# Kernel optimization log

Hardware: AMD Instinct MI355X
Metric: run time of the kernel (lower is better)

## Reference

```python
import jax, jax.numpy as jnp
import numpy as np

MARGIN = 1.0
EPS = 1e-08


def setup_inputs() -> dict:
    key = jax.random.key(0)
    k0, k1 = jax.random.split(key)
    kernels0 = jax.random.normal(k0, (2048, 3, 3), dtype=jnp.float32)
    kernels1 = jax.random.normal(k1, (1024, 5, 5), dtype=jnp.float32)
    return {"kernels0": kernels0, "kernels1": kernels1}


def _layer_loss(kernels):
    n, d, _ = kernels.shape
    # Frobenius-normalize each kernel
    norms = jnp.sqrt(jnp.sum(kernels * kernels, axis=(1, 2), keepdims=True)) + EPS
    kn = kernels / norms                      # (n, d, d)
    inv = jnp.linalg.inv(kn)                  # (n, d, d)
    # AB[i, j] = inv[i] @ kn[j]; BA[i, j] = inv[j] @ kn[i]
    ab = jnp.einsum('iab,jbc->ijac', inv, kn)  # (n, n, d, d)
    ba = jnp.einsum('jab,ibc->ijac', inv, kn)  # (n, n, d, d)
    eye = jnp.eye(d, dtype=kernels.dtype)
    diff_ab = jnp.sqrt(jnp.sum((eye - ab) ** 2, axis=(2, 3)))  # (n, n)
    diff_ba = jnp.sqrt(jnp.sum((eye - ba) ** 2, axis=(2, 3)))  # (n, n)
    combined = jnp.tril(diff_ab) + jnp.triu(diff_ba)
    loss_mat = jax.nn.relu(MARGIN - combined)
    mask = ~jnp.eye(n, dtype=bool)
    loss_mat = jnp.where(mask, loss_mat, 0.0)
    return jnp.sum(loss_mat) / (n * (n - 1))


def reference(kernels0, kernels1):
    losses = [_layer_loss(kernels0), _layer_loss(kernels1)]
    return sum(losses) / len(losses)
```

## Files before the change

kernel.cpp:

```cpp
#include <hip/hip_runtime.h>
#include <math.h>

#define N0 2048
#define N1 1024
#define T0 128
#define T1 64
#define M0 (N0 / T0)
#define M1 (N1 / T1)
#define NB0 (M0 * (M0 + 1) / 2)
#define NB1 (M1 * (M1 + 1) / 2)
#define NBTOT (NB0 + NB1)


__device__ __forceinline__ void inv3_newton(const float* __restrict__ src, float* __restrict__ out) {
    float a[9];
    float ss = 0.0f;
#pragma unroll
    for (int e = 0; e < 9; ++e) { a[e] = src[e]; ss = fmaf(a[e], a[e], ss); }
    float rn = 1.0f / (sqrtf(ss) + 1e-8f);
#pragma unroll
    for (int e = 0; e < 9; ++e) a[e] *= rn;
    float c00 = a[4] * a[8] - a[5] * a[7];
    float c01 = -(a[3] * a[8] - a[5] * a[6]);
    float c02 = a[3] * a[7] - a[4] * a[6];
    float det = a[0] * c00 + a[1] * c01 + a[2] * c02;
    float id = 1.0f / det;
    float x[9];
    x[0] = c00 * id;
    x[1] = (a[2] * a[7] - a[1] * a[8]) * id;
    x[2] = (a[1] * a[5] - a[2] * a[4]) * id;
    x[3] = c01 * id;
    x[4] = (a[0] * a[8] - a[2] * a[6]) * id;
    x[5] = (a[2] * a[3] - a[0] * a[5]) * id;
    x[6] = c02 * id;
    x[7] = (a[1] * a[6] - a[0] * a[7]) * id;
    x[8] = (a[0] * a[4] - a[1] * a[3]) * id;
    float r[9];
#pragma unroll
    for (int i = 0; i < 3; ++i)
#pragma unroll
        for (int j = 0; j < 3; ++j) {
            float m = a[i * 3 + 0] * x[j];
            m = fmaf(a[i * 3 + 1], x[3 + j], m);
            m = fmaf(a[i * 3 + 2], x[6 + j], m);
            r[i * 3 + j] = ((i == j) ? 2.0f : 0.0f) - m;
        }
#pragma unroll
    for (int i = 0; i < 3; ++i)
#pragma unroll
        for (int j = 0; j < 3; ++j) {
            float m = x[i * 3 + 0] * r[j];
            m = fmaf(x[i * 3 + 1], r[3 + j], m);
            m = fmaf(x[i * 3 + 2], r[6 + j], m);
            out[i * 3 + j] = m;
        }
}

__device__ __forceinline__ void norm3(const float* __restrict__ src, float* __restrict__ out) {
    float a[9];
    float ss = 0.0f;
#pragma unroll
    for (int e = 0; e < 9; ++e) { a[e] = src[e]; ss = fmaf(a[e], a[e], ss); }
    float rn = 1.0f / (sqrtf(ss) + 1e-8f);
#pragma unroll
    for (int e = 0; e < 9; ++e) out[e] = a[e] * rn;
}

__device__ __forceinline__ void inv5_newton(const float* __restrict__ src, float* __restrict__ out) {
    float A[5][5], B[5][5], K[5][5];
    float ss = 0.0f;
#pragma unroll
    for (int r = 0; r < 5; ++r)
#pragma unroll
        for (int c = 0; c < 5; ++c) {
            float v = src[r * 5 + c];
            A[r][c] = v;
            ss = fmaf(v, v, ss);
        }
    float rn = 1.0f / (sqrtf(ss) + 1e-8f);
#pragma unroll
    for (int r = 0; r < 5; ++r)
#pragma unroll
        for (int c = 0; c < 5; ++c) {
            A[r][c] *= rn;
            K[r][c] = A[r][c];
            B[r][c] = (r == c) ? 1.0f : 0.0f;
        }
#pragma unroll
    for (int k = 0; k < 5; ++k) {
#pragma unroll
        for (int r = k + 1; r < 5; ++r) {
            bool sw = fabsf(A[r][k]) > fabsf(A[k][k]);
#pragma unroll
            for (int c = k; c < 5; ++c) {
                float Ar = A[r][c], Ak = A[k][c];
                A[r][c] = sw ? Ak : Ar;
                A[k][c] = sw ? Ar : Ak;
            }
#pragma unroll
            for (int c = 0; c < 5; ++c) {
                float Br = B[r][c], Bk = B[k][c];
                B[r][c] = sw ? Bk : Br;
                B[k][c] = sw ? Br : Bk;
            }
        }
        float piv = 1.0f / A[k][k];
#pragma unroll
        for (int c = k; c < 5; ++c) A[k][c] *= piv;
#pragma unroll
        for (int c = 0; c < 5; ++c) B[k][c] *= piv;
#pragma unroll
        for (int r = 0; r < 5; ++r) {
            if (r == k) continue;
            float f = A[r][k];
#pragma unroll
            for (int c = k; c < 5; ++c) A[r][c] = fmaf(-f, A[k][c], A[r][c]);
#pragma unroll
            for (int c = 0; c < 5; ++c) B[r][c] = fmaf(-f, B[k][c], B[r][c]);
        }
    }
    float R[5][5];
#pragma unroll
    for (int i = 0; i < 5; ++i)
#pragma unroll
        for (int j = 0; j < 5; ++j) {
            float m = K[i][0] * B[0][j];
#pragma unroll
            for (int k = 1; k < 5; ++k) m = fmaf(K[i][k], B[k][j], m);
            R[i][j] = ((i == j) ? 2.0f : 0.0f) - m;
        }
#pragma unroll
    for (int i = 0; i < 5; ++i)
#pragma unroll
        for (int j = 0; j < 5; ++j) {
            float m = B[i][0] * R[0][j];
#pragma unroll
            for (int k = 1; k < 5; ++k) m = fmaf(B[i][k], R[k][j], m);
            out[i * 5 + j] = m;
        }
}

__device__ __forceinline__ void norm5(const float* __restrict__ src, float* __restrict__ out) {
    float a[25];
    float ss = 0.0f;
#pragma unroll
    for (int e = 0; e < 25; ++e) { a[e] = src[e]; ss = fmaf(a[e], a[e], ss); }
    float rn = 1.0f / (sqrtf(ss) + 1e-8f);
#pragma unroll
    for (int e = 0; e < 25; ++e) out[e] = a[e] * rn;
}

__device__ __forceinline__ void tri_decode(int t, int& bi, int& bj) {
    bi = (int)((sqrtf(8.0f * t + 1.0f) - 1.0f) * 0.5f);
    while ((bi + 1) * (bi + 2) / 2 <= t) ++bi;
    while (bi * (bi + 1) / 2 > t) --bi;
    bj = t - bi * (bi + 1) / 2;
}

__global__ __launch_bounds__(256) void fused_kernel(const float* __restrict__ k0,
                                                    const float* __restrict__ k1,
                                                    float* __restrict__ out) {
    __shared__ float sA[1600];
    __shared__ float sB[1600];
    int tid = threadIdx.x;
    float contrib = 0.0f;
    bool isL0 = blockIdx.x < NB0;

    if (isL0) {
        int bi, bj;
        tri_decode(blockIdx.x, bi, bj);
        if (tid < 128) {
            inv3_newton(&k0[(bi * T0 + tid) * 9], &sA[tid * 9]);
        } else {
            int m = tid - 128;
            norm3(&k0[(bj * T0 + m) * 9], &sB[m * 9]);
        }
        __syncthreads();

        int ty = tid >> 4, tx = tid & 15;
        int ibase = bi * T0 + ty * 8, jbase = bj * T0 + tx * 8;
        float a[8][9];
#pragma unroll
        for (int u = 0; u < 8; ++u)
#pragma unroll
            for (int e = 0; e < 9; ++e) a[u][e] = sA[(ty * 8 + u) * 9 + e];
#pragma unroll
        for (int v = 0; v < 8; ++v) {
            float b[9];
#pragma unroll
            for (int e = 0; e < 9; ++e) b[e] = sB[(tx * 8 + v) * 9 + e];
#pragma unroll
            for (int u = 0; u < 8; ++u) {
                float s = 0.0f;
#pragma unroll
                for (int r = 0; r < 3; ++r)
#pragma unroll
                    for (int c = 0; c < 3; ++c) {
                        float m = a[u][r * 3 + 0] * b[c];
                        m = fmaf(a[u][r * 3 + 1], b[3 + c], m);
                        m = fmaf(a[u][r * 3 + 2], b[6 + c], m);
                        float d = ((r == c) ? 1.0f : 0.0f) - m;
                        s = fmaf(d, d, s);
                    }
                bool take = ((ibase + u) > (jbase + v)) && (s < 1.0f);
                contrib += take ? (1.0f - sqrtf(s)) : 0.0f;
            }
        }
    } else {
        int bi, bj;
        tri_decode(blockIdx.x - NB0, bi, bj);
        if (tid < 64) {
            inv5_newton(&k1[(bi * T1 + tid) * 25], &sA[tid * 25]);
        } else if (tid < 128) {
            int m = tid - 64;
            norm5(&k1[(bj * T1 + m) * 25], &sB[m * 25]);
        }
        __syncthreads();

        int ty = tid >> 4, tx = tid & 15;
        int ibase = bi * T1 + ty * 4, jbase = bj * T1 + tx * 4;
        float a[4][25];
#pragma unroll
        for (int u = 0; u < 4; ++u)
#pragma unroll
            for (int e = 0; e < 25; ++e) a[u][e] = sA[(ty * 4 + u) * 25 + e];
#pragma unroll
        for (int v = 0; v < 4; ++v) {
            float b[25];
#pragma unroll
            for (int e = 0; e < 25; ++e) b[e] = sB[(tx * 4 + v) * 25 + e];
#pragma unroll
            for (int u = 0; u < 4; ++u) {
                float s = 0.0f;
#pragma unroll
                for (int r = 0; r < 5; ++r)
#pragma unroll
                    for (int c = 0; c < 5; ++c) {
                        float m = a[u][r * 5 + 0] * b[c];
#pragma unroll
                        for (int k = 1; k < 5; ++k) m = fmaf(a[u][r * 5 + k], b[k * 5 + c], m);
                        float d = ((r == c) ? 1.0f : 0.0f) - m;
                        s = fmaf(d, d, s);
                    }
                bool take = ((ibase + u) > (jbase + v)) && (s < 1.0f);
                contrib += take ? (1.0f - sqrtf(s)) : 0.0f;
            }
        }
    }

#pragma unroll
    for (int off = 32; off; off >>= 1) contrib += __shfl_down(contrib, off);
    __shared__ float wsum[4];
    if ((tid & 63) == 0) wsum[tid >> 6] = contrib;
    __syncthreads();
    if (tid == 0) {
        double part = (double)(wsum[0] + wsum[1] + wsum[2] + wsum[3]);
        double scale = isL0 ? 1.0 / ((double)N0 * (double)(N0 - 1))
                            : 1.0 / ((double)N1 * (double)(N1 - 1));
        unsafeAtomicAdd(out, (float)(part * scale));
    }
}

extern "C" void kernel_launch(void* const* d_in, const int* in_sizes, int n_in,
                              void* d_out, int out_size, void* d_ws, size_t ws_size,
                              hipStream_t stream) {
    const float* k0 = (const float*)d_in[0];
    const float* k1 = (const float*)d_in[1];
    float* out = (float*)d_out;
    (void)d_ws; (void)ws_size;

    fused_kernel<<<NBTOT, 256, 0, stream>>>(k0, k1, out);
}
```

Baseline: 71.80 us.

## Precompute normalized kernels and inverses in a prep kernel; stride tile rows

Kernel normalization and inversion move out of the pairwise kernel into a separate prep kernel that writes normalized kernels and inverses to workspace once. Each pair block then only copies its tiles into shared memory, instead of recomputing the Newton-refined inverse for its row tile on every block. The per-thread row and column mapping also changes from contiguous groups of 8 or 4 to a stride of 16, which alters the shared-memory bank access pattern. The cost is an extra kernel launch and a global-memory round trip for the precomputed data.

Measured after the change: 75.73 us. 1.05x slower.

```diff
diff --git a/kernel.cpp b/kernel.cpp
--- a/kernel.cpp
+++ b/kernel.cpp
@@ -12,142 +12,134 @@
 #define NBTOT (NB0 + NB1)
 
 
-__device__ __forceinline__ void inv3_newton(const float* __restrict__ src, float* __restrict__ out) {
-    float a[9];
-    float ss = 0.0f;
-#pragma unroll
-    for (int e = 0; e < 9; ++e) { a[e] = src[e]; ss = fmaf(a[e], a[e], ss); }
-    float rn = 1.0f / (sqrtf(ss) + 1e-8f);
-#pragma unroll
-    for (int e = 0; e < 9; ++e) a[e] *= rn;
-    float c00 = a[4] * a[8] - a[5] * a[7];
-    float c01 = -(a[3] * a[8] - a[5] * a[6]);
-    float c02 = a[3] * a[7] - a[4] * a[6];
-    float det = a[0] * c00 + a[1] * c01 + a[2] * c02;
-    float id = 1.0f / det;
-    float x[9];
-    x[0] = c00 * id;
-    x[1] = (a[2] * a[7] - a[1] * a[8]) * id;
-    x[2] = (a[1] * a[5] - a[2] * a[4]) * id;
-    x[3] = c01 * id;
-    x[4] = (a[0] * a[8] - a[2] * a[6]) * id;
-    x[5] = (a[2] * a[3] - a[0] * a[5]) * id;
-    x[6] = c02 * id;
-    x[7] = (a[1] * a[6] - a[0] * a[7]) * id;
-    x[8] = (a[0] * a[4] - a[1] * a[3]) * id;
-    float r[9];
-#pragma unroll
-    for (int i = 0; i < 3; ++i)
-#pragma unroll
-        for (int j = 0; j < 3; ++j) {
-            float m = a[i * 3 + 0] * x[j];
-            m = fmaf(a[i * 3 + 1], x[3 + j], m);
-            m = fmaf(a[i * 3 + 2], x[6 + j], m);
-            r[i * 3 + j] = ((i == j) ? 2.0f : 0.0f) - m;
-        }
-#pragma unroll
-    for (int i = 0; i < 3; ++i)
-#pragma unroll
-        for (int j = 0; j < 3; ++j) {
-            float m = x[i * 3 + 0] * r[j];
-            m = fmaf(x[i * 3 + 1], r[3 + j], m);
-            m = fmaf(x[i * 3 + 2], r[6 + j], m);
-            out[i * 3 + j] = m;
-        }
-}
-
-__device__ __forceinline__ void norm3(const float* __restrict__ src, float* __restrict__ out) {
-    float a[9];
-    float ss = 0.0f;
-#pragma unroll
-    for (int e = 0; e < 9; ++e) { a[e] = src[e]; ss = fmaf(a[e], a[e], ss); }
-    float rn = 1.0f / (sqrtf(ss) + 1e-8f);
-#pragma unroll
-    for (int e = 0; e < 9; ++e) out[e] = a[e] * rn;
-}
-
-__device__ __forceinline__ void inv5_newton(const float* __restrict__ src, float* __restrict__ out) {
-    float A[5][5], B[5][5], K[5][5];
-    float ss = 0.0f;
-#pragma unroll
-    for (int r = 0; r < 5; ++r)
-#pragma unroll
-        for (int c = 0; c < 5; ++c) {
-            float v = src[r * 5 + c];
-            A[r][c] = v;
-            ss = fmaf(v, v, ss);
-        }
-    float rn = 1.0f / (sqrtf(ss) + 1e-8f);
-#pragma unroll
-    for (int r = 0; r < 5; ++r)
-#pragma unroll
-        for (int c = 0; c < 5; ++c) {
-            A[r][c] *= rn;
-            K[r][c] = A[r][c];
-            B[r][c] = (r == c) ? 1.0f : 0.0f;
-        }
-#pragma unroll
-    for (int k = 0; k < 5; ++k) {
-#pragma unroll
-        for (int r = k + 1; r < 5; ++r) {
-            bool sw = fabsf(A[r][k]) > fabsf(A[k][k]);
-#pragma unroll
-            for (int c = k; c < 5; ++c) {
-                float Ar = A[r][c], Ak = A[k][c];
-                A[r][c] = sw ? Ak : Ar;
-                A[k][c] = sw ? Ar : Ak;
-            }
-#pragma unroll
-            for (int c = 0; c < 5; ++c) {
-                float Br = B[r][c], Bk = B[k][c];
-                B[r][c] = sw ? Bk : Br;
-                B[k][c] = sw ? Br : Bk;
-            }
-        }
-        float piv = 1.0f / A[k][k];
-#pragma unroll
-        for (int c = k; c < 5; ++c) A[k][c] *= piv;
-#pragma unroll
-        for (int c = 0; c < 5; ++c) B[k][c] *= piv;
-#pragma unroll
-        for (int r = 0; r < 5; ++r) {
-            if (r == k) continue;
-            float f = A[r][k];
-#pragma unroll
-            for (int c = k; c < 5; ++c) A[r][c] = fmaf(-f, A[k][c], A[r][c]);
-#pragma unroll
-            for (int c = 0; c < 5; ++c) B[r][c] = fmaf(-f, B[k][c], B[r][c]);
+__global__ __launch_bounds__(64) void prep_kernel(const float* __restrict__ k0,
+                                                  const float* __restrict__ k1,
+                                                  float* __restrict__ kn0,
+                                                  float* __restrict__ inv0,
+                                                  float* __restrict__ kn1,
+                                                  float* __restrict__ inv1) {
+    int t = blockIdx.x * blockDim.x + threadIdx.x;
+    if (t < N0) {
+        float a[9];
+        float ss = 0.0f;
+#pragma unroll
+        for (int e = 0; e < 9; ++e) { a[e] = k0[t * 9 + e]; ss = fmaf(a[e], a[e], ss); }
+        float rn = 1.0f / (sqrtf(ss) + 1e-8f);
+#pragma unroll
+        for (int e = 0; e < 9; ++e) a[e] *= rn;
+        float c00 = a[4] * a[8] - a[5] * a[7];
+        float c01 = -(a[3] * a[8] - a[5] * a[6]);
+        float c02 = a[3] * a[7] - a[4] * a[6];
+        float det = a[0] * c00 + a[1] * c01 + a[2] * c02;
+        float id = 1.0f / det;
+        float x[9];
+        x[0] = c00 * id;
+        x[1] = (a[2] * a[7] - a[1] * a[8]) * id;
+        x[2] = (a[1] * a[5] - a[2] * a[4]) * id;
+        x[3] = c01 * id;
+        x[4] = (a[0] * a[8] - a[2] * a[6]) * id;
+        x[5] = (a[2] * a[3] - a[0] * a[5]) * id;
+        x[6] = c02 * id;
+        x[7] = (a[1] * a[6] - a[0] * a[7]) * id;
+        x[8] = (a[0] * a[4] - a[1] * a[3]) * id;
+        float r[9];
+#pragma unroll
+        for (int i = 0; i < 3; ++i)
+#pragma unroll
+            for (int j = 0; j < 3; ++j) {
+                float m = a[i * 3 + 0] * x[j];
+                m = fmaf(a[i * 3 + 1], x[3 + j], m);
+                m = fmaf(a[i * 3 + 2], x[6 + j], m);
+                r[i * 3 + j] = ((i == j) ? 2.0f : 0.0f) - m;
+            }
+#pragma unroll
+        for (int i = 0; i < 3; ++i)
+#pragma unroll
+            for (int j = 0; j < 3; ++j) {
+                float m = x[i * 3 + 0] * r[j];
+                m = fmaf(x[i * 3 + 1], r[3 + j], m);
+                m = fmaf(x[i * 3 + 2], r[6 + j], m);
+                inv0[t * 9 + i * 3 + j] = m;
+            }
+#pragma unroll
+        for (int e = 0; e < 9; ++e) kn0[t * 9 + e] = a[e];
+    } else {
+        int u = t - N0;
+        if (u < N1) {
+            float A[5][5], B[5][5], K[5][5];
+            float ss = 0.0f;
+#pragma unroll
+            for (int r = 0; r < 5; ++r)
+#pragma unroll
+                for (int c = 0; c < 5; ++c) {
+                    float v = k1[u * 25 + r * 5 + c];
+                    A[r][c] = v;
+                    ss = fmaf(v, v, ss);
+                }
+            float rn = 1.0f / (sqrtf(ss) + 1e-8f);
+#pragma unroll
+            for (int r = 0; r < 5; ++r)
+#pragma unroll
+                for (int c = 0; c < 5; ++c) {
+                    A[r][c] *= rn;
+                    K[r][c] = A[r][c];
+                    kn1[u * 25 + r * 5 + c] = A[r][c];
+                    B[r][c] = (r == c) ? 1.0f : 0.0f;
+                }
+#pragma unroll
+            for (int k = 0; k < 5; ++k) {
+#pragma unroll
+                for (int r = k + 1; r < 5; ++r) {
+                    bool sw = fabsf(A[r][k]) > fabsf(A[k][k]);
+#pragma unroll
+                    for (int c = k; c < 5; ++c) {
+                        float Ar = A[r][c], Ak = A[k][c];
+                        A[r][c] = sw ? Ak : Ar;
+                        A[k][c] = sw ? Ar : Ak;
+                    }
+#pragma unroll
+                    for (int c = 0; c < 5; ++c) {
+                        float Br = B[r][c], Bk = B[k][c];
+                        B[r][c] = sw ? Bk : Br;
+                        B[k][c] = sw ? Br : Bk;
+                    }
+                }
+                float piv = 1.0f / A[k][k];
+#pragma unroll
+                for (int c = k; c < 5; ++c) A[k][c] *= piv;
+#pragma unroll
+                for (int c = 0; c < 5; ++c) B[k][c] *= piv;
+#pragma unroll
+                for (int r = 0; r < 5; ++r) {
+                    if (r == k) continue;
+                    float f = A[r][k];
+#pragma unroll
+                    for (int c = k; c < 5; ++c) A[r][c] = fmaf(-f, A[k][c], A[r][c]);
+#pragma unroll
+                    for (int c = 0; c < 5; ++c) B[r][c] = fmaf(-f, B[k][c], B[r][c]);
+                }
+            }
+            float R[5][5];
+#pragma unroll
+            for (int i = 0; i < 5; ++i)
+#pragma unroll
+                for (int j = 0; j < 5; ++j) {
+                    float m = K[i][0] * B[0][j];
+#pragma unroll
+                    for (int k = 1; k < 5; ++k) m = fmaf(K[i][k], B[k][j], m);
+                    R[i][j] = ((i == j) ? 2.0f : 0.0f) - m;
+                }
+#pragma unroll
+            for (int i = 0; i < 5; ++i)
+#pragma unroll
+                for (int j = 0; j < 5; ++j) {
+                    float m = B[i][0] * R[0][j];
+#pragma unroll
+                    for (int k = 1; k < 5; ++k) m = fmaf(B[i][k], R[k][j], m);
+                    inv1[u * 25 + i * 5 + j] = m;
+                }
         }
     }
-    float R[5][5];
-#pragma unroll
-    for (int i = 0; i < 5; ++i)
-#pragma unroll
-        for (int j = 0; j < 5; ++j) {
-            float m = K[i][0] * B[0][j];
-#pragma unroll
-            for (int k = 1; k < 5; ++k) m = fmaf(K[i][k], B[k][j], m);
-            R[i][j] = ((i == j) ? 2.0f : 0.0f) - m;
-        }
-#pragma unroll
-    for (int i = 0; i < 5; ++i)
-#pragma unroll
-        for (int j = 0; j < 5; ++j) {
-            float m = B[i][0] * R[0][j];
-#pragma unroll
-            for (int k = 1; k < 5; ++k) m = fmaf(B[i][k], R[k][j], m);
-            out[i * 5 + j] = m;
-        }
-}
-
-__device__ __forceinline__ void norm5(const float* __restrict__ src, float* __restrict__ out) {
-    float a[25];
-    float ss = 0.0f;
-#pragma unroll
-    for (int e = 0; e < 25; ++e) { a[e] = src[e]; ss = fmaf(a[e], a[e], ss); }
-    float rn = 1.0f / (sqrtf(ss) + 1e-8f);
-#pragma unroll
-    for (int e = 0; e < 25; ++e) out[e] = a[e] * rn;
 }
 
 __device__ __forceinline__ void tri_decode(int t, int& bi, int& bj) {
@@ -157,8 +149,10 @@
     bj = t - bi * (bi + 1) / 2;
 }
 
-__global__ __launch_bounds__(256) void fused_kernel(const float* __restrict__ k0,
-                                                    const float* __restrict__ k1,
+__global__ __launch_bounds__(256) void pairs_kernel(const float* __restrict__ inv0,
+                                                    const float* __restrict__ kn0,
+                                                    const float* __restrict__ inv1,
+                                                    const float* __restrict__ kn1,
                                                     float* __restrict__ out) {
     __shared__ float sA[1600];
     __shared__ float sB[1600];
@@ -169,26 +163,24 @@
     if (isL0) {
         int bi, bj;
         tri_decode(blockIdx.x, bi, bj);
-        if (tid < 128) {
-            inv3_newton(&k0[(bi * T0 + tid) * 9], &sA[tid * 9]);
-        } else {
-            int m = tid - 128;
-            norm3(&k0[(bj * T0 + m) * 9], &sB[m * 9]);
+        for (int e = tid; e < T0 * 9; e += 256) {
+            sA[e] = inv0[bi * (T0 * 9) + e];
+            sB[e] = kn0[bj * (T0 * 9) + e];
         }
         __syncthreads();
 
         int ty = tid >> 4, tx = tid & 15;
-        int ibase = bi * T0 + ty * 8, jbase = bj * T0 + tx * 8;
         float a[8][9];
 #pragma unroll
         for (int u = 0; u < 8; ++u)
 #pragma unroll
-            for (int e = 0; e < 9; ++e) a[u][e] = sA[(ty * 8 + u) * 9 + e];
+            for (int e = 0; e < 9; ++e) a[u][e] = sA[(ty + 16 * u) * 9 + e];
 #pragma unroll
         for (int v = 0; v < 8; ++v) {
             float b[9];
 #pragma unroll
-            for (int e = 0; e < 9; ++e) b[e] = sB[(tx * 8 + v) * 9 + e];
+            for (int e = 0; e < 9; ++e) b[e] = sB[(tx + 16 * v) * 9 + e];
+            int j = bj * T0 + tx + 16 * v;
 #pragma unroll
             for (int u = 0; u < 8; ++u) {
                 float s = 0.0f;
@@ -202,33 +194,32 @@
                         float d = ((r == c) ? 1.0f : 0.0f) - m;
                         s = fmaf(d, d, s);
                     }
-                bool take = ((ibase + u) > (jbase + v)) && (s < 1.0f);
+                int i = bi * T0 + ty + 16 * u;
+                bool take = (i > j) && (s < 1.0f);
                 contrib += take ? (1.0f - sqrtf(s)) : 0.0f;
             }
         }
     } else {
         int bi, bj;
         tri_decode(blockIdx.x - NB0, bi, bj);
-        if (tid < 64) {
-            inv5_newton(&k1[(bi * T1 + tid) * 25], &sA[tid * 25]);
-        } else if (tid < 128) {
-            int m = tid - 64;
-            norm5(&k1[(bj * T1 + m) * 25], &sB[m * 25]);
+        for (int e = tid; e < T1 * 25; e += 256) {
+            sA[e] = inv1[bi * (T1 * 25) + e];
+            sB[e] = kn1[bj * (T1 * 25) + e];
         }
         __syncthreads();
 
         int ty = tid >> 4, tx = tid & 15;
-        int ibase = bi * T1 + ty * 4, jbase = bj * T1 + tx * 4;
         float a[4][25];
 #pragma unroll
         for (int u = 0; u < 4; ++u)
 #pragma unroll
-            for (int e = 0; e < 25; ++e) a[u][e] = sA[(ty * 4 + u) * 25 + e];
+            for (int e = 0; e < 25; ++e) a[u][e] = sA[(ty + 16 * u) * 25 + e];
 #pragma unroll
         for (int v = 0; v < 4; ++v) {
             float b[25];
 #pragma unroll
-            for (int e = 0; e < 25; ++e) b[e] = sB[(tx * 4 + v) * 25 + e];
+            for (int e = 0; e < 25; ++e) b[e] = sB[(tx + 16 * v) * 25 + e];
+            int j = bj * T1 + tx + 16 * v;
 #pragma unroll
             for (int u = 0; u < 4; ++u) {
                 float s = 0.0f;
@@ -242,7 +233,8 @@
                         float d = ((r == c) ? 1.0f : 0.0f) - m;
                         s = fmaf(d, d, s);
                     }
-                bool take = ((ibase + u) > (jbase + v)) && (s < 1.0f);
+                int i = bi * T1 + ty + 16 * u;
+                bool take = (i > j) && (s < 1.0f);
                 contrib += take ? (1.0f - sqrtf(s)) : 0.0f;
             }
         }
@@ -267,7 +259,15 @@
     const float* k0 = (const float*)d_in[0];
     const float* k1 = (const float*)d_in[1];
     float* out = (float*)d_out;
-    (void)d_ws; (void)ws_size;
-
-    fused_kernel<<<NBTOT, 256, 0, stream>>>(k0, k1, out);
-}
+
+    float* ws = (float*)d_ws;
+    float* kn0 = ws;
+    float* inv0 = kn0 + N0 * 9;
+    float* kn1 = inv0 + N0 * 9;
+    float* inv1 = kn1 + N1 * 25;
+
+    int totalPrep = N0 + N1;
+    prep_kernel<<<(totalPrep + 63) / 64, 64, 0, stream>>>(k0, k1, kn0, inv0, kn1, inv1);
+
+    pairs_kernel<<<NBTOT, 256, 0, stream>>>(inv0, kn0, inv1, kn1, out);
+}
```
